# Kernel tuning notes

Measured on AMD Instinct MI355X. Metric: run time of the kernel, lower is better.

## Reference

```python
import jax, jax.numpy as jnp
import numpy as np

N = 100000
E = 1600000
H, C = 4, 64
NEG_SLOPE = 0.2


def setup_inputs() -> dict:
    key = jax.random.key(0)
    ks = jax.random.split(key, 12)
    def rn(k, shape, scale=1.0):
        return jax.random.normal(k, shape, dtype=jnp.float32) * scale
    return {
        "x": rn(ks[0], (N, 3)),
        "edge_index": jax.random.randint(ks[1], (2, E), 0, N, dtype=jnp.int64),
        "W1": rn(ks[2], (3, H * C), 0.5),
        "a_src1": rn(ks[3], (H, C), 0.1),
        "a_dst1": rn(ks[4], (H, C), 0.1),
        "b1": jnp.zeros((H * C,), jnp.float32),
        "W2": rn(ks[5], (H * C, H * C), 0.06),
        "a_src2": rn(ks[6], (H, C), 0.1),
        "a_dst2": rn(ks[7], (H, C), 0.1),
        "b2": jnp.zeros((H * C,), jnp.float32),
        "fc_w": rn(ks[8], (H * C, 2), 0.06),
        "fc_b": jnp.zeros((2,), jnp.float32),
    }


def _gat_layer(x, src, dst, W, a_src, a_dst, bias):
    # x: [N, F_in] -> h: [N, H, C]
    h = (x @ W).reshape(N, H, C)
    # per-node attention logits
    al_src = jnp.einsum("nhc,hc->nh", h, a_src)  # [N, H]
    al_dst = jnp.einsum("nhc,hc->nh", h, a_dst)  # [N, H]
    e = jax.nn.leaky_relu(al_src[src] + al_dst[dst], NEG_SLOPE)  # [E', H]
    # segment softmax over incoming edges of each dst node
    m = jax.ops.segment_max(e, dst, num_segments=N)  # [N, H]
    m = jnp.where(jnp.isfinite(m), m, 0.0)
    ex = jnp.exp(e - m[dst])
    denom = jax.ops.segment_sum(ex, dst, num_segments=N)  # [N, H]
    alpha = ex / (denom[dst] + 1e-16)  # [E', H]
    # scatter-aggregate messages
    out = jax.ops.segment_sum(h[src] * alpha[:, :, None], dst, num_segments=N)
    return out.reshape(N, H * C) + bias


def reference(x, edge_index, W1, a_src1, a_dst1, b1, W2, a_src2, a_dst2, b2, fc_w, fc_b):
    # add self-loops (PyG GATConv default)
    loop = jnp.arange(N, dtype=edge_index.dtype)
    src = jnp.concatenate([edge_index[0], loop])
    dst = jnp.concatenate([edge_index[1], loop])
    h = _gat_layer(x, src, dst, W1, a_src1, a_dst1, b1)
    h = jax.nn.relu(h)
    h = _gat_layer(h, src, dst, W2, a_src2, a_dst2, b2)
    h = jax.nn.relu(h)
    return h @ fc_w + fc_b
```

## Files before the change

### kernel.cpp

```cpp
#include <hip/hip_runtime.h>

#define NN 100000
#define NE 1600000
#define HC 256
#define NBUCK 391
#define CHUNK 8192

typedef __attribute__((ext_vector_type(8))) short short8;
typedef __attribute__((ext_vector_type(4))) float f32x4;

__device__ __forceinline__ float4 ld4(const float* p) { return *(const float4*)p; }
__device__ __forceinline__ unsigned short f2bf(float f) {
    unsigned u = __float_as_uint(f);
    return (unsigned short)((u + 0x7fffu + ((u >> 16) & 1u)) >> 16);
}
__device__ __forceinline__ float bf2f(unsigned short h) { return __uint_as_float(((unsigned)h) << 16); }

__device__ __forceinline__ void unpack8(uint4 v, float* f) {
    f[0] = __uint_as_float(v.x << 16); f[1] = __uint_as_float(v.x & 0xffff0000u);
    f[2] = __uint_as_float(v.y << 16); f[3] = __uint_as_float(v.y & 0xffff0000u);
    f[4] = __uint_as_float(v.z << 16); f[5] = __uint_as_float(v.z & 0xffff0000u);
    f[6] = __uint_as_float(v.w << 16); f[7] = __uint_as_float(v.w & 0xffff0000u);
}

__global__ __launch_bounds__(256) void k_bhist(const int* __restrict__ dst,
                                               int* __restrict__ bhist) {
    __shared__ int h[NBUCK];
    int t = threadIdx.x;
    for (int j = t; j < NBUCK; j += 256) h[j] = 0;
    __syncthreads();
    int base = blockIdx.x * 2048;
    int lim = min(base + 2048, NE);
    for (int i = base + t; i < lim; i += 256)
        atomicAdd(&h[dst[i] >> 8], 1);
    __syncthreads();
    for (int j = t; j < NBUCK; j += 256) if (h[j]) atomicAdd(&bhist[j], h[j]);
}

__global__ void k_bscan(const int* __restrict__ bhist, int* __restrict__ boffs,
                        int* __restrict__ bcursor, int* __restrict__ offs) {
    __shared__ int sh[512];
    int t = threadIdx.x;
    int v = (t < NBUCK) ? bhist[t] : 0;
    sh[t] = v;
    __syncthreads();
    for (int o = 1; o < 512; o <<= 1) {
        int y = (t >= o) ? sh[t - o] : 0;
        __syncthreads();
        sh[t] += y;
        __syncthreads();
    }
    if (t < NBUCK) { int e = sh[t] - v; boffs[t] = e; bcursor[t] = e; }
    if (t == 0) { boffs[NBUCK] = NE; offs[NN] = NE; }
}

__global__ __launch_bounds__(256) void k_bscatter2(
    const int* __restrict__ src, const int* __restrict__ dst,
    int* __restrict__ bcursor, int2* __restrict__ eb) {
    __shared__ int lh[NBUCK];
    __shared__ unsigned short lrank[CHUNK];
    int t = threadIdx.x;
    int base = blockIdx.x * CHUNK;
    int lim = min(base + CHUNK, NE);
    for (int j = t; j < NBUCK; j += 256) lh[j] = 0;
    __syncthreads();
    for (int i = base + t; i < lim; i += 256)
        lrank[i - base] = (unsigned short)atomicAdd(&lh[dst[i] >> 8], 1);
    __syncthreads();
    for (int j = t; j < NBUCK; j += 256) {
        int c = lh[j];
        lh[j] = c ? atomicAdd(&bcursor[j], c) : 0;
    }
    __syncthreads();
    for (int i = base + t; i < lim; i += 256) {
        int d = dst[i];
        int p = lh[d >> 8] + lrank[i - base];
        eb[p] = make_int2(src[i], d);
    }
}

__global__ __launch_bounds__(256) void k_bsort(const int2* __restrict__ eb,
                                               const int* __restrict__ boffs,
                                               int* __restrict__ offs,
                                               int* __restrict__ csr) {
    __shared__ int hist[256];
    __shared__ int sc[256];
    int b = blockIdx.x, t = threadIdx.x;
    int beg = boffs[b], end = boffs[b + 1];
    hist[t] = 0;
    __syncthreads();
    for (int i = beg + t; i < end; i += 256)
        atomicAdd(&hist[eb[i].y & 255], 1);
    __syncthreads();
    int v = hist[t];
    sc[t] = v;
    __syncthreads();
    for (int o = 1; o < 256; o <<= 1) {
        int y = (t >= o) ? sc[t - o] : 0;
        __syncthreads();
        sc[t] += y;
        __syncthreads();
    }
    int mypos = beg + sc[t] - v;
    int gd = b * 256 + t;
    if (gd < NN) offs[gd] = mypos;
    __syncthreads();
    hist[t] = mypos;
    __syncthreads();
    for (int i = beg + t; i < end; i += 256) {
        int2 e = eb[i];
        int p = atomicAdd(&hist[e.y & 255], 1);
        csr[p] = e.x;
    }
}

__global__ void k_prep_p1(const float* __restrict__ W1, const float* __restrict__ as1,
                          const float* __restrict__ ad1, float* __restrict__ ps1,
                          float* __restrict__ pd1) {
    int t = threadIdx.x;
    int h = t >> 6, cc = t & 63;
    float avs = as1[h * 64 + cc], avd = ad1[h * 64 + cc];
    for (int k = 0; k < 3; ++k) {
        float w = W1[k * 256 + h * 64 + cc];
        float vs = w * avs, vd = w * avd;
        #pragma unroll
        for (int m = 1; m < 64; m <<= 1) { vs += __shfl_xor(vs, m, 64); vd += __shfl_xor(vd, m, 64); }
        if (cc == 0) { ps1[h * 4 + k] = vs; pd1[h * 4 + k] = vd; }
    }
}

__global__ void k_prep_bt(const float* __restrict__ W2, unsigned short* __restrict__ Bt) {
    int vk = blockIdx.x, c = threadIdx.x;
    float v = W2[(size_t)(vk & 255) * HC + c];
    unsigned short hi = f2bf(v);
    unsigned short o = (vk < 256) ? hi : f2bf(v - bf2f(hi));
    Bt[(size_t)c * 512 + vk] = o;
}

__global__ __launch_bounds__(256) void k_agg1(
    const float* __restrict__ x, const float* __restrict__ W1,
    const float* __restrict__ ps1, const float* __restrict__ pd1,
    const int* __restrict__ offs, const int* __restrict__ csr,
    const float* __restrict__ b1, unsigned short* __restrict__ zh) {
    __shared__ float Y[16][16];
    int t = threadIdx.x;
    int g = t >> 4, l16 = t & 15;
    int d = blockIdx.x * 16 + g;
    float ps[4][3], pd[4][3];
    #pragma unroll
    for (int h = 0; h < 4; ++h) {
        ps[h][0] = ps1[h * 4 + 0]; ps[h][1] = ps1[h * 4 + 1]; ps[h][2] = ps1[h * 4 + 2];
        pd[h][0] = pd1[h * 4 + 0]; pd[h][1] = pd1[h * 4 + 1]; pd[h][2] = pd1[h * 4 + 2];
    }
    float xd0 = x[d * 3], xd1 = x[d * 3 + 1], xd2 = x[d * 3 + 2];
    float ald[4];
    #pragma unroll
    for (int h = 0; h < 4; ++h) ald[h] = xd0 * pd[h][0] + xd1 * pd[h][1] + xd2 * pd[h][2];
    float S[4] = {0.f, 0.f, 0.f, 0.f};
    float X0[4] = {0.f, 0.f, 0.f, 0.f}, X1[4] = {0.f, 0.f, 0.f, 0.f}, X2[4] = {0.f, 0.f, 0.f, 0.f};
    int beg = offs[d], end = offs[d + 1];
    for (int idx = beg + l16; idx < end; idx += 16) {
        int sn = csr[idx] * 3;
        float a0 = x[sn], a1 = x[sn + 1], a2 = x[sn + 2];
        #pragma unroll
        for (int h = 0; h < 4; ++h) {
            float e = a0 * ps[h][0] + a1 * ps[h][1] + a2 * ps[h][2] + ald[h];
            e = e > 0.f ? e : 0.2f * e;
            float p = __expf(e);
            S[h] += p; X0[h] += p * a0; X1[h] += p * a1; X2[h] += p * a2;
        }
    }
    if (l16 == 0) {
        #pragma unroll
        for (int h = 0; h < 4; ++h) {
            float e = xd0 * ps[h][0] + xd1 * ps[h][1] + xd2 * ps[h][2] + ald[h];
            e = e > 0.f ? e : 0.2f * e;
            float p = __expf(e);
            S[h] += p; X0[h] += p * xd0; X1[h] += p * xd1; X2[h] += p * xd2;
        }
    }
    #pragma unroll
    for (int m = 1; m < 16; m <<= 1) {
        #pragma unroll
        for (int h = 0; h < 4; ++h) {
            S[h] += __shfl_xor(S[h], m, 64);
            X0[h] += __shfl_xor(X0[h], m, 64);
            X1[h] += __shfl_xor(X1[h], m, 64);
            X2[h] += __shfl_xor(X2[h], m, 64);
        }
    }
    if (l16 == 0) {
        *(float4*)&Y[g][0]  = make_float4(S[0], S[1], S[2], S[3]);
        *(float4*)&Y[g][4]  = make_float4(X0[0], X0[1], X0[2], X0[3]);
        *(float4*)&Y[g][8]  = make_float4(X1[0], X1[1], X1[2], X1[3]);
        *(float4*)&Y[g][12] = make_float4(X2[0], X2[1], X2[2], X2[3]);
    }
    __syncthreads();
    int lane = t & 63, w = t >> 6;
    int head = lane >> 4, c = lane << 2;
    float4 w0 = ld4(W1 + c), w1 = ld4(W1 + 256 + c), w2 = ld4(W1 + 512 + c);
    float4 bv = ld4(b1 + c);
    #pragma unroll
    for (int rr = 0; rr < 4; ++rr) {
        int g2 = w * 4 + rr;
        int d2 = blockIdx.x * 16 + g2;
        float inv = 1.f / Y[g2][head];
        float Y0 = Y[g2][4 + head] * inv;
        float Y1 = Y[g2][8 + head] * inv;
        float Y2 = Y[g2][12 + head] * inv;
        float4 z;
        z.x = fmaxf(Y0 * w0.x + Y1 * w1.x + Y2 * w2.x + bv.x, 0.f);
        z.y = fmaxf(Y0 * w0.y + Y1 * w1.y + Y2 * w2.y + bv.y, 0.f);
        z.z = fmaxf(Y0 * w0.z + Y1 * w1.z + Y2 * w2.z + bv.z, 0.f);
        z.w = fmaxf(Y0 * w0.w + Y1 * w1.w + Y2 * w2.w + bv.w, 0.f);
        ushort4 hi;
        hi.x = f2bf(z.x); hi.y = f2bf(z.y); hi.z = f2bf(z.z); hi.w = f2bf(z.w);
        *(ushort4*)(zh + (size_t)d2 * HC + c) = hi;
    }
}

__global__ __launch_bounds__(512) void k_gemm2_mfma(
    const unsigned short* __restrict__ zh, const unsigned short* __restrict__ Bt,
    const float* __restrict__ a_s, const float* __restrict__ a_d,
    unsigned short* __restrict__ h2bf, float* __restrict__ alS2,
    float* __restrict__ alD2) {
    __shared__ __align__(16) unsigned short As[128 * 64];
    __shared__ __align__(16) unsigned short Bs[256 * 64];
    int t = threadIdx.x;
    int l = t & 63, w = t >> 6;
    int wm = w >> 2, wn = w & 3;
    int lr = l & 15, lk = l >> 4;
    int row0 = blockIdx.x * 128;

    f32x4 acc[4][4];
    f32x4 z4 = {0.f, 0.f, 0.f, 0.f};
    #pragma unroll
    for (int i = 0; i < 4; ++i)
        #pragma unroll
        for (int j = 0; j < 4; ++j) acc[i][j] = z4;

    int sa_row = t >> 2, sa_q = t & 3;
    const unsigned short* zrow = zh + (size_t)(row0 + sa_row) * HC;
    bool a_ok = (row0 + sa_row) < NN;
    int sb_col = t >> 1, sb_h = t & 1;
    const unsigned short* btrow = Bt + (size_t)sb_col * 512;

    for (int kt = 0; kt < 8; ++kt) {
        int ksb = kt * 64;
        int acol0 = ksb & 255;
        uint4 av0 = make_uint4(0, 0, 0, 0), av1 = make_uint4(0, 0, 0, 0);
        if (a_ok) {
            av0 = *(const uint4*)(zrow + acol0 + sa_q * 16);
            av1 = *(const uint4*)(zrow + acol0 + sa_q * 16 + 8);
        }
        int rs = sa_row * 64;
        *(uint4*)&As[rs + ((2 * sa_q) ^ (sa_row & 7)) * 8] = av0;
        *(uint4*)&As[rs + ((2 * sa_q + 1) ^ (sa_row & 7)) * 8] = av1;
        const unsigned short* bsrc = btrow + ksb + sb_h * 32;
        int cs = sb_col * 64;
        #pragma unroll
        for (int j = 0; j < 4; ++j) {
            uint4 bv = *(const uint4*)(bsrc + j * 8);
            *(uint4*)&Bs[cs + ((sb_h * 4 + j) ^ (sb_col & 7)) * 8] = bv;
        }
        __syncthreads();
        #pragma unroll
        for (int s = 0; s < 2; ++s) {
            short8 af[4], bfr[4];
            #pragma unroll
            for (int fi = 0; fi < 4; ++fi) {
                int row = wm * 64 + fi * 16 + lr;
                int kg = (s * 4 + lk) ^ (row & 7);
                af[fi] = *(const short8*)&As[row * 64 + kg * 8];
            }
            #pragma unroll
            for (int bj = 0; bj < 4; ++bj) {
                int col = wn * 64 + bj * 16 + lr;
                int kg = (s * 4 + lk) ^ (col & 7);
                bfr[bj] = *(const short8*)&Bs[col * 64 + kg * 8];
            }
            #pragma unroll
            for (int fi = 0; fi < 4; ++fi)
                #pragma unroll
                for (int bj = 0; bj < 4; ++bj)
                    acc[fi][bj] = __builtin_amdgcn_mfma_f32_16x16x32_bf16(af[fi], bfr[bj], acc[fi][bj], 0, 0, 0);
        }
        __syncthreads();
    }

    float asr[4], adr[4];
    #pragma unroll
    for (int bj = 0; bj < 4; ++bj) {
        int cc = wn * 64 + bj * 16 + lr;
        asr[bj] = a_s[cc];
        adr[bj] = a_d[cc];
    }
    #pragma unroll
    for (int fi = 0; fi < 4; ++fi) {
        #pragma unroll
        for (int r = 0; r < 4; ++r) {
            int grow = row0 + wm * 64 + fi * 16 + lk * 4 + r;
            bool ok = grow < NN;
            float ps = 0.f, pd = 0.f;
            #pragma unroll
            for (int bj = 0; bj < 4; ++bj) {
                float vv = acc[fi][bj][r];
                if (ok) h2bf[(size_t)grow * HC + wn * 64 + bj * 16 + lr] = f2bf(vv);
                ps += vv * asr[bj];
                pd += vv * adr[bj];
            }
            #pragma unroll
            for (int mm = 1; mm < 16; mm <<= 1) {
                ps += __shfl_xor(ps, mm, 64);
                pd += __shfl_xor(pd, mm, 64);
            }
            if (ok && lr == 0) {
                alS2[grow * 4 + wn] = ps;
                alD2[grow * 4 + wn] = pd;
            }
        }
    }
}

__global__ __launch_bounds__(256) void k_prep_p(
    const float* __restrict__ alS2, const float* __restrict__ alD2,
    const int* __restrict__ offs, const int* __restrict__ csr,
    float* __restrict__ pw) {
    int gt = blockIdx.x * blockDim.x + threadIdx.x;
    int d = gt >> 4;
    int l16 = threadIdx.x & 15;
    int head = l16 & 3;
    int eo = l16 >> 2;
    float ad = alD2[d * 4 + head];
    int beg = offs[d], end = offs[d + 1];
    for (int idx = beg + eo; idx < end; idx += 4) {
        int sn = csr[idx];
        float e = alS2[sn * 4 + head] + ad;
        e = e > 0.f ? e : 0.2f * e;
        pw[(size_t)idx * 4 + head] = __expf(e);
    }
}

__global__ __launch_bounds__(256) void k_agg2(
    const unsigned short* __restrict__ h2bf, const float* __restrict__ alS2,
    const float* __restrict__ alD2, const int* __restrict__ offs,
    const int* __restrict__ csr, const float* __restrict__ pw,
    const float* __restrict__ b2, const float* __restrict__ fcw,
    const float* __restrict__ fcb, float* __restrict__ out) {
    int gt = blockIdx.x * blockDim.x + threadIdx.x;
    int d = gt >> 4;
    int l16 = threadIdx.x & 15;
    int head = l16 >> 2;
    int cb = l16 * 16;
    float e0 = alS2[d * 4 + head] + alD2[d * 4 + head];
    e0 = e0 > 0.f ? e0 : 0.2f * e0;
    float s = __expf(e0);
    float acc[16], f[16];
    {
        const uint4* rp = (const uint4*)(h2bf + (size_t)d * HC + cb);
        uint4 r0 = rp[0], r1 = rp[1];
        unpack8(r0, f); unpack8(r1, f + 8);
        #pragma unroll
        for (int j = 0; j < 16; ++j) acc[j] = s * f[j];
    }
    int beg = offs[d], end = offs[d + 1];
    if (beg < end) {
        int i1 = (beg + 1 < end) ? beg + 1 : beg;
        int sn0 = csr[beg];
        float pv0 = pw[(size_t)beg * 4 + head];
        const uint4* rp0 = (const uint4*)(h2bf + (size_t)sn0 * HC + cb);
        uint4 a0 = rp0[0], b0 = rp0[1];
        int sn1 = csr[i1];
        float pv1 = (beg + 1 < end) ? pw[(size_t)(beg + 1) * 4 + head] : 0.f;
        const uint4* rp1 = (const uint4*)(h2bf + (size_t)sn1 * HC + cb);
        uint4 a1 = rp1[0], b1v = rp1[1];
        for (int i = beg; i < end; ++i) {
            int nx = i + 2;
            bool okn = nx < end;
            int snn = okn ? csr[nx] : sn0;
            float pvn = okn ? pw[(size_t)nx * 4 + head] : 0.f;
            const uint4* rpn = (const uint4*)(h2bf + (size_t)snn * HC + cb);
            uint4 an = rpn[0], bn = rpn[1];
            unpack8(a0, f); unpack8(b0, f + 8);
            s += pv0;
            #pragma unroll
            for (int j = 0; j < 16; ++j) acc[j] += pv0 * f[j];
            a0 = a1; b0 = b1v; pv0 = pv1;
            a1 = an; b1v = bn; pv1 = pvn;
        }
    }
    float inv = 1.f / (s + 1e-16f);
    float p0 = 0.f, p1 = 0.f;
    #pragma unroll
    for (int q = 0; q < 4; ++q) {
        float4 bv = ld4(b2 + cb + q * 4);
        float4 fa = ld4(fcw + (cb + q * 4) * 2);
        float4 fb = ld4(fcw + (cb + q * 4) * 2 + 4);
        float o0 = fmaxf(acc[q * 4 + 0] * inv + bv.x, 0.f);
        float o1 = fmaxf(acc[q * 4 + 1] * inv + bv.y, 0.f);
        float o2 = fmaxf(acc[q * 4 + 2] * inv + bv.z, 0.f);
        float o3 = fmaxf(acc[q * 4 + 3] * inv + bv.w, 0.f);
        p0 += o0 * fa.x + o1 * fa.z + o2 * fb.x + o3 * fb.z;
        p1 += o0 * fa.y + o1 * fa.w + o2 * fb.y + o3 * fb.w;
    }
    #pragma unroll
    for (int mm = 1; mm < 16; mm <<= 1) {
        p0 += __shfl_xor(p0, mm, 64);
        p1 += __shfl_xor(p1, mm, 64);
    }
    if (l16 == 0) {
        out[d * 2 + 0] = p0 + fcb[0];
        out[d * 2 + 1] = p1 + fcb[1];
    }
}

extern "C" void kernel_launch(void* const* d_in, const int* in_sizes, int n_in,
                              void* d_out, int out_size, void* d_ws, size_t ws_size,
                              hipStream_t stream) {
    const float* x   = (const float*)d_in[0];
    const int*   ei  = (const int*)d_in[1];
    const float* W1  = (const float*)d_in[2];
    const float* as1 = (const float*)d_in[3];
    const float* ad1 = (const float*)d_in[4];
    const float* b1  = (const float*)d_in[5];
    const float* W2  = (const float*)d_in[6];
    const float* as2 = (const float*)d_in[7];
    const float* ad2 = (const float*)d_in[8];
    const float* b2  = (const float*)d_in[9];
    const float* fcw = (const float*)d_in[10];
    const float* fcb = (const float*)d_in[11];
    float* out = (float*)d_out;

    char* p = (char*)d_ws;
    unsigned short* zh   = (unsigned short*)p; p += (size_t)NN * HC * 2;
    unsigned short* h2bf = (unsigned short*)p; p += (size_t)NN * HC * 2;
    float* alS2 = (float*)p; p += (size_t)NN * 4 * 4;
    float* alD2 = (float*)p; p += (size_t)NN * 4 * 4;
    float* ps1  = (float*)p; p += 256;
    float* pd1  = (float*)p; p += 256;
    unsigned short* Bt = (unsigned short*)p; p += (size_t)256 * 512 * 2;
    int* offs   = (int*)p;   p += (size_t)(NN + 2) * 4;
    int* csr    = (int*)p;   p += (size_t)NE * 4;
    int2* eb    = (int2*)p;  p += (size_t)NE * 8;
    float* pw   = (float*)p; p += (size_t)NE * 4 * 4;
    int* bhist  = (int*)p;   p += 2048;
    int* boffs  = (int*)p;   p += 2048;
    int* bcursor= (int*)p;   p += 2048;

    const int* e_src = ei;
    const int* e_dst = ei + NE;

    hipMemsetAsync(bhist, 0, NBUCK * sizeof(int), stream);
    k_bhist<<<(NE + 2047) / 2048, 256, 0, stream>>>(e_dst, bhist);
    k_bscan<<<1, 512, 0, stream>>>(bhist, boffs, bcursor, offs);
    k_bscatter2<<<(NE + CHUNK - 1) / CHUNK, 256, 0, stream>>>(e_src, e_dst, bcursor, eb);
    k_bsort<<<NBUCK, 256, 0, stream>>>(eb, boffs, offs, csr);

    k_prep_bt<<<512, 256, 0, stream>>>(W2, Bt);
    k_prep_p1<<<1, 256, 0, stream>>>(W1, as1, ad1, ps1, pd1);

    k_agg1<<<NN / 16, 256, 0, stream>>>(x, W1, ps1, pd1, offs, csr, b1, zh);
    k_gemm2_mfma<<<(NN + 127) / 128, 512, 0, stream>>>(zh, Bt, as2, ad2, h2bf, alS2, alD2);
    k_prep_p<<<NN / 16, 256, 0, stream>>>(alS2, alD2, offs, csr, pw);
    k_agg2<<<NN / 16, 256, 0, stream>>>(h2bf, alS2, alD2, offs, csr, pw, b2,
                                        fcw, fcb, out);
}
```

Before: 309.1 us.

## Fuse edge-weight computation into agg2 and register-prefetch GEMM tiles

```diff
diff --git a/kernel.cpp b/kernel.cpp
--- a/kernel.cpp
+++ b/kernel.cpp
@@ -244,26 +244,39 @@
     bool a_ok = (row0 + sa_row) < NN;
     int sb_col = t >> 1, sb_h = t & 1;
     const unsigned short* btrow = Bt + (size_t)sb_col * 512;
+    int rs = sa_row * 64;
+    int cs = sb_col * 64;
+
+    uint4 av0 = make_uint4(0, 0, 0, 0), av1 = av0;
+    uint4 bvr[4];
+    if (a_ok) {
+        av0 = *(const uint4*)(zrow + sa_q * 16);
+        av1 = *(const uint4*)(zrow + sa_q * 16 + 8);
+    }
+    #pragma unroll
+    for (int j = 0; j < 4; ++j)
+        bvr[j] = *(const uint4*)(btrow + sb_h * 32 + j * 8);
+    *(uint4*)&As[rs + ((2 * sa_q) ^ (sa_row & 7)) * 8] = av0;
+    *(uint4*)&As[rs + ((2 * sa_q + 1) ^ (sa_row & 7)) * 8] = av1;
+    #pragma unroll
+    for (int j = 0; j < 4; ++j)
+        *(uint4*)&Bs[cs + ((sb_h * 4 + j) ^ (sb_col & 7)) * 8] = bvr[j];
+    __syncthreads();
 
     for (int kt = 0; kt < 8; ++kt) {
-        int ksb = kt * 64;
-        int acol0 = ksb & 255;
-        uint4 av0 = make_uint4(0, 0, 0, 0), av1 = make_uint4(0, 0, 0, 0);
-        if (a_ok) {
-            av0 = *(const uint4*)(zrow + acol0 + sa_q * 16);
-            av1 = *(const uint4*)(zrow + acol0 + sa_q * 16 + 8);
-        }
-        int rs = sa_row * 64;
-        *(uint4*)&As[rs + ((2 * sa_q) ^ (sa_row & 7)) * 8] = av0;
-        *(uint4*)&As[rs + ((2 * sa_q + 1) ^ (sa_row & 7)) * 8] = av1;
-        const unsigned short* bsrc = btrow + ksb + sb_h * 32;
-        int cs = sb_col * 64;
-        #pragma unroll
-        for (int j = 0; j < 4; ++j) {
-            uint4 bv = *(const uint4*)(bsrc + j * 8);
-            *(uint4*)&Bs[cs + ((sb_h * 4 + j) ^ (sb_col & 7)) * 8] = bv;
-        }
-        __syncthreads();
+        uint4 nav0 = make_uint4(0, 0, 0, 0), nav1 = nav0, nbv[4];
+        nbv[0] = nbv[1] = nbv[2] = nbv[3] = nav0;
+        if (kt < 7) {
+            int ksb = (kt + 1) * 64;
+            int acol0 = ksb & 255;
+            if (a_ok) {
+                nav0 = *(const uint4*)(zrow + acol0 + sa_q * 16);
+                nav1 = *(const uint4*)(zrow + acol0 + sa_q * 16 + 8);
+            }
+            const unsigned short* bsrc = btrow + ksb + sb_h * 32;
+            #pragma unroll
+            for (int j = 0; j < 4; ++j) nbv[j] = *(const uint4*)(bsrc + j * 8);
+        }
         #pragma unroll
         for (int s = 0; s < 2; ++s) {
             short8 af[4], bfr[4];
@@ -284,6 +297,14 @@
                 #pragma unroll
                 for (int bj = 0; bj < 4; ++bj)
                     acc[fi][bj] = __builtin_amdgcn_mfma_f32_16x16x32_bf16(af[fi], bfr[bj], acc[fi][bj], 0, 0, 0);
+        }
+        __syncthreads();
+        if (kt < 7) {
+            *(uint4*)&As[rs + ((2 * sa_q) ^ (sa_row & 7)) * 8] = nav0;
+            *(uint4*)&As[rs + ((2 * sa_q + 1) ^ (sa_row & 7)) * 8] = nav1;
+            #pragma unroll
+            for (int j = 0; j < 4; ++j)
+                *(uint4*)&Bs[cs + ((sb_h * 4 + j) ^ (sb_col & 7)) * 8] = nbv[j];
         }
         __syncthreads();
     }
@@ -322,37 +343,19 @@
     }
 }
 
-__global__ __launch_bounds__(256) void k_prep_p(
-    const float* __restrict__ alS2, const float* __restrict__ alD2,
-    const int* __restrict__ offs, const int* __restrict__ csr,
-    float* __restrict__ pw) {
-    int gt = blockIdx.x * blockDim.x + threadIdx.x;
-    int d = gt >> 4;
-    int l16 = threadIdx.x & 15;
-    int head = l16 & 3;
-    int eo = l16 >> 2;
-    float ad = alD2[d * 4 + head];
-    int beg = offs[d], end = offs[d + 1];
-    for (int idx = beg + eo; idx < end; idx += 4) {
-        int sn = csr[idx];
-        float e = alS2[sn * 4 + head] + ad;
-        e = e > 0.f ? e : 0.2f * e;
-        pw[(size_t)idx * 4 + head] = __expf(e);
-    }
-}
-
 __global__ __launch_bounds__(256) void k_agg2(
     const unsigned short* __restrict__ h2bf, const float* __restrict__ alS2,
     const float* __restrict__ alD2, const int* __restrict__ offs,
-    const int* __restrict__ csr, const float* __restrict__ pw,
-    const float* __restrict__ b2, const float* __restrict__ fcw,
-    const float* __restrict__ fcb, float* __restrict__ out) {
+    const int* __restrict__ csr, const float* __restrict__ b2,
+    const float* __restrict__ fcw, const float* __restrict__ fcb,
+    float* __restrict__ out) {
     int gt = blockIdx.x * blockDim.x + threadIdx.x;
     int d = gt >> 4;
     int l16 = threadIdx.x & 15;
     int head = l16 >> 2;
     int cb = l16 * 16;
-    float e0 = alS2[d * 4 + head] + alD2[d * 4 + head];
+    float ald = alD2[d * 4 + head];
+    float e0 = alS2[d * 4 + head] + ald;
     e0 = e0 > 0.f ? e0 : 0.2f * e0;
     float s = __expf(e0);
     float acc[16], f[16];
@@ -367,26 +370,29 @@
     if (beg < end) {
         int i1 = (beg + 1 < end) ? beg + 1 : beg;
         int sn0 = csr[beg];
-        float pv0 = pw[(size_t)beg * 4 + head];
+        float la0 = alS2[sn0 * 4 + head];
         const uint4* rp0 = (const uint4*)(h2bf + (size_t)sn0 * HC + cb);
         uint4 a0 = rp0[0], b0 = rp0[1];
         int sn1 = csr[i1];
-        float pv1 = (beg + 1 < end) ? pw[(size_t)(beg + 1) * 4 + head] : 0.f;
+        float la1 = (beg + 1 < end) ? alS2[sn1 * 4 + head] : -1e30f;
         const uint4* rp1 = (const uint4*)(h2bf + (size_t)sn1 * HC + cb);
         uint4 a1 = rp1[0], b1v = rp1[1];
         for (int i = beg; i < end; ++i) {
             int nx = i + 2;
             bool okn = nx < end;
             int snn = okn ? csr[nx] : sn0;
-            float pvn = okn ? pw[(size_t)nx * 4 + head] : 0.f;
+            float lan = okn ? alS2[snn * 4 + head] : -1e30f;
             const uint4* rpn = (const uint4*)(h2bf + (size_t)snn * HC + cb);
             uint4 an = rpn[0], bn = rpn[1];
+            float e = la0 + ald;
+            e = e > 0.f ? e : 0.2f * e;
+            float pv = __expf(e);
             unpack8(a0, f); unpack8(b0, f + 8);
-            s += pv0;
-            #pragma unroll
-            for (int j = 0; j < 16; ++j) acc[j] += pv0 * f[j];
-            a0 = a1; b0 = b1v; pv0 = pv1;
-            a1 = an; b1v = bn; pv1 = pvn;
+            s += pv;
+            #pragma unroll
+            for (int j = 0; j < 16; ++j) acc[j] += pv * f[j];
+            a0 = a1; b0 = b1v; la0 = la1;
+            a1 = an; b1v = bn; la1 = lan;
         }
     }
     float inv = 1.f / (s + 1e-16f);
@@ -442,7 +448,6 @@
     int* offs   = (int*)p;   p += (size_t)(NN + 2) * 4;
     int* csr    = (int*)p;   p += (size_t)NE * 4;
     int2* eb    = (int2*)p;  p += (size_t)NE * 8;
-    float* pw   = (float*)p; p += (size_t)NE * 4 * 4;
     int* bhist  = (int*)p;   p += 2048;
     int* boffs  = (int*)p;   p += 2048;
     int* bcursor= (int*)p;   p += 2048;
@@ -461,7 +466,6 @@
 
     k_agg1<<<NN / 16, 256, 0, stream>>>(x, W1, ps1, pd1, offs, csr, b1, zh);
     k_gemm2_mfma<<<(NN + 127) / 128, 512, 0, stream>>>(zh, Bt, as2, ad2, h2bf, alS2, alD2);
-    k_prep_p<<<NN / 16, 256, 0, stream>>>(alS2, alD2, offs, csr, pw);
-    k_agg2<<<NN / 16, 256, 0, stream>>>(h2bf, alS2, alD2, offs, csr, pw, b2,
+    k_agg2<<<NN / 16, 256, 0, stream>>>(h2bf, alS2, alD2, offs, csr, b2,
                                         fcw, fcb, out);
 }
```

Result: slower. 324.8 us (+5.1%).
